# Optimization experiments

Measured on AMD Instinct MI355X. Metric: run time of the kernel, lower is better.

The kernel has to match this reference:

```python
import jax, jax.numpy as jnp
import numpy as np

# Qwen3-Next-like dims
B, S, HID = 2, 2048, 2048
H, KV, D, ROT = 16, 2, 128, 32
G = H // KV              # kv repeat groups
SCALE = D ** -0.5
EPS = 1e-6
BETA_BIAS, BIAS_CAP = 1.0, 3.0   # L1 logit bias
BETA_POST = 0.5                  # L2 post-softmax rescale
ALPHA_K, ALPHA_V = 0.1, 0.1      # L4 k/v rescale
GMIN, GMAX = 0.9, 1.1
EMIN, EMAX = 0.9, 1.1


def setup_inputs() -> dict:
    key = jax.random.key(0)
    ks = jax.random.split(key, 10)
    hidden_states = jax.random.normal(ks[0], (B, S, HID), jnp.float32)
    # partial rotary embeddings (rot_dim = head_dim // 4)
    pos = jnp.arange(S, dtype=jnp.float32)
    inv = 1.0 / (10000.0 ** (jnp.arange(0, ROT, 2, dtype=jnp.float32) / ROT))
    freqs = pos[:, None] * inv[None, :]
    emb = jnp.concatenate([freqs, freqs], axis=-1)          # [S, ROT]
    cos = jnp.broadcast_to(jnp.cos(emb)[None], (B, S, ROT)).astype(jnp.float32)
    sin = jnp.broadcast_to(jnp.sin(emb)[None], (B, S, ROT)).astype(jnp.float32)
    # additive causal mask [B,1,S,S]
    causal = jnp.tril(jnp.ones((S, S), jnp.bool_))
    attention_mask = jnp.where(causal, 0.0, -1e9).astype(jnp.float32)
    attention_mask = jnp.broadcast_to(attention_mask[None, None], (B, 1, S, S))
    # key prior: positive, sums to 1 over kv_len
    prior = jax.nn.softmax(jax.random.normal(ks[1], (S,), jnp.float32))
    s = 0.02
    Wq = jax.random.normal(ks[2], (HID, H * D * 2), jnp.float32) * s
    Wk = jax.random.normal(ks[3], (HID, KV * D), jnp.float32) * s
    Wv = jax.random.normal(ks[4], (HID, KV * D), jnp.float32) * s
    Wo = jax.random.normal(ks[5], (H * D, HID), jnp.float32) * s
    q_norm_w = 1.0 + 0.02 * jax.random.normal(ks[6], (D,), jnp.float32)
    k_norm_w = 1.0 + 0.02 * jax.random.normal(ks[7], (D,), jnp.float32)
    return {"hidden_states": hidden_states, "cos": cos, "sin": sin,
            "attention_mask": attention_mask, "prior": prior,
            "Wq": Wq, "Wk": Wk, "Wv": Wv, "Wo": Wo,
            "q_norm_w": q_norm_w, "k_norm_w": k_norm_w}


def _rms(x, w):
    return x * jax.lax.rsqrt(jnp.mean(x * x, axis=-1, keepdims=True) + EPS) * w


def _rot_half(x):
    x1, x2 = jnp.split(x, 2, axis=-1)
    return jnp.concatenate([-x2, x1], axis=-1)


def _rope(x, cos, sin):
    # x: [B,h,S,D]; rotary on first ROT dims only (Qwen3-Next partial rotary)
    xr, xp = x[..., :ROT], x[..., ROT:]
    xr = xr * cos + _rot_half(xr) * sin
    return jnp.concatenate([xr, xp], axis=-1)


def reference(hidden_states, cos, sin, attention_mask, prior, Wq, Wk, Wv, Wo, q_norm_w, k_norm_w):
    h = hidden_states
    # gated q projection: chunk into query + gate
    qg = (h @ Wq).reshape(B, S, H, 2 * D)
    q, gate = qg[..., :D], qg[..., D:]
    gate = gate.reshape(B, S, H * D)
    q = _rms(q, q_norm_w).transpose(0, 2, 1, 3)                       # [B,H,S,D]
    k = _rms((h @ Wk).reshape(B, S, KV, D), k_norm_w).transpose(0, 2, 1, 3)  # [B,KV,S,D]
    v = (h @ Wv).reshape(B, S, KV, D).transpose(0, 2, 1, 3)
    c, s_ = cos[:, None], sin[:, None]                                # [B,1,S,ROT]
    q, k = _rope(q, c, s_), _rope(k, c, s_)
    k = jnp.repeat(k, G, axis=1)                                      # GQA expand -> [B,H,S,D]
    v = jnp.repeat(v, G, axis=1)
    # L4: prior-based elementwise k/v rescale with clamped gamma/eta
    pc = prior * S                                                    # mean ~1 over keys
    gamma = jnp.clip(1.0 + ALPHA_K * (pc - 1.0), GMIN, GMAX)
    eta = jnp.clip(1.0 + ALPHA_V * (pc - 1.0), EMIN, EMAX)
    k = k * gamma[None, None, :, None]
    v = v * eta[None, None, :, None]
    scores = jnp.einsum('bhqd,bhkd->bhqk', q, k) * SCALE
    # L1: capped steering bias on logits
    scores = scores + jnp.clip(BETA_BIAS * prior, -BIAS_CAP, BIAS_CAP)[None, None, None, :]
    scores = scores + attention_mask
    probs = jax.nn.softmax(scores.astype(jnp.float32), axis=-1)       # fp32 softmax
    # L2: post-softmax prior rescale + renorm
    p2 = probs * (1.0 + BETA_POST * pc)[None, None, None, :]
    probs = p2 / jnp.sum(p2, axis=-1, keepdims=True)
    out = jnp.einsum('bhqk,bhkd->bhqd', probs.astype(h.dtype), v)
    out = out.transpose(0, 2, 1, 3).reshape(B, S, H * D)
    out = out * jax.nn.sigmoid(gate)                                  # gated attention output
    return out @ Wo
```

## Files before the change

kernel.cpp:

```cpp
#include <hip/hip_runtime.h>
#include <hip/hip_bf16.h>
#include <stdint.h>

#define B_    2
#define S_    2048
#define HID_  2048
#define H_    16
#define KV_   2
#define D_    128
#define ROT_  32
#define QGS   4608
#define SCALE_ 0.08838834764831845f

typedef __attribute__((ext_vector_type(8))) short  short8;
typedef __attribute__((ext_vector_type(4))) float  floatx4;

__device__ __forceinline__ float b2f(unsigned short u) {
  union { unsigned int i; float f; } v; v.i = ((unsigned int)u) << 16; return v.f;
}
__device__ __forceinline__ unsigned short f2b(float f) {
  union { float f; unsigned int i; } v; v.f = f;
  return (unsigned short)((v.i + 0x7fffu + ((v.i >> 16) & 1u)) >> 16);
}
__device__ __forceinline__ void gload_lds16(const unsigned short* g, unsigned short* l) {
  __builtin_amdgcn_global_load_lds((const __attribute__((address_space(1))) void*)g,
                                   (__attribute__((address_space(3))) void*)l, 16, 0, 0);
}

__device__ __forceinline__ void transpose_body(const float* __restrict__ in,
                                               unsigned short* __restrict__ out,
                                               int R, int C, int bx, int by, int t) {
  __shared__ unsigned short tile[64][68];
  int tx = t & 15, ty = t >> 4;
  long c0 = (long)bx * 64, r0 = (long)by * 64;
#pragma unroll
  for (int i = 0; i < 4; i++) {
    int row = ty + 16 * i;
    const float* src = in + (r0 + row) * C + c0 + 4 * tx;
    float4 v = *(const float4*)src;
    tile[row][4 * tx + 0] = f2b(v.x);
    tile[row][4 * tx + 1] = f2b(v.y);
    tile[row][4 * tx + 2] = f2b(v.z);
    tile[row][4 * tx + 3] = f2b(v.w);
  }
  __syncthreads();
#pragma unroll
  for (int i = 0; i < 4; i++) {
    int oc = ty + 16 * i;
    ushort4 v;
    v.x = tile[4 * tx + 0][oc];
    v.y = tile[4 * tx + 1][oc];
    v.z = tile[4 * tx + 2][oc];
    v.w = tile[4 * tx + 3][oc];
    *(ushort4*)(out + (c0 + oc) * R + r0 + 4 * tx) = v;
  }
}

__global__ __launch_bounds__(256) void k_preproc(const float* __restrict__ h_f,
                                                 const float* __restrict__ prior,
                                                 const float* __restrict__ Wq,
                                                 const float* __restrict__ Wk,
                                                 const float* __restrict__ Wv,
                                                 const float* __restrict__ Wo,
                                                 unsigned short* __restrict__ hb,
                                                 unsigned short* __restrict__ WqkvT,
                                                 unsigned short* __restrict__ WoT,
                                                 float* __restrict__ ge,
                                                 float* __restrict__ kbias) {
  int bx = blockIdx.x;
  const int t = threadIdx.x;
  if (bx < 8) {
    int i = bx * 256 + t;
    float p  = prior[i];
    float pc = p * (float)S_;
    float g  = 1.0f + 0.1f * (pc - 1.0f);
    g = fminf(fmaxf(g, 0.9f), 1.1f);
    ge[i] = g;
    float cb = fminf(fmaxf(p, -3.0f), 3.0f);
    kbias[i] = cb + logf(1.0f + 0.5f * pc);
    return;
  }
  bx -= 8;
  if (bx < 4096) {
    long i0 = ((long)bx * 256 + t) * 8;
    float4 a = *(const float4*)(h_f + i0);
    float4 b = *(const float4*)(h_f + i0 + 4);
    short8 v;
    v[0] = (short)f2b(a.x); v[1] = (short)f2b(a.y);
    v[2] = (short)f2b(a.z); v[3] = (short)f2b(a.w);
    v[4] = (short)f2b(b.x); v[5] = (short)f2b(b.y);
    v[6] = (short)f2b(b.z); v[7] = (short)f2b(b.w);
    *(short8*)(hb + i0) = v;
    return;
  }
  bx -= 4096;
  if (bx < 2048) { transpose_body(Wq, WqkvT, 2048, 4096, bx & 63, bx >> 6, t); return; }
  bx -= 2048;
  if (bx < 1024) { transpose_body(Wo, WoT, 2048, 2048, bx & 31, bx >> 5, t); return; }
  bx -= 1024;
  if (bx < 128)  { transpose_body(Wk, WqkvT + (size_t)4096 * 2048, 2048, 256, bx & 3, bx >> 2, t); return; }
  bx -= 128;
  transpose_body(Wv, WqkvT + (size_t)4352 * 2048, 2048, 256, bx & 3, bx >> 2, t);
}

template <int OUT32>
__global__ __launch_bounds__(256) void k_gemm_bt(const unsigned short* __restrict__ A,
                                                 const unsigned short* __restrict__ Bt,
                                                 void* __restrict__ Cv,
                                                 int M, int N, int K) {
  __shared__ __align__(16) unsigned short As[2][128 * 32];
  __shared__ __align__(16) unsigned short Bs[2][128 * 32];
  const int t    = threadIdx.x;
  const int lane = t & 63;
  const int wv   = t >> 6;
  const int wm   = wv >> 1, wn = wv & 1;
  const int nwg  = gridDim.x * gridDim.y;
  const int orig = blockIdx.y * gridDim.x + blockIdx.x;
  const int wg   = (orig & 7) * (nwg >> 3) + (orig >> 3);
  const int bxx  = wg % gridDim.x, byy = wg / gridDim.x;
  const long m0  = (long)byy * 128;
  const long n0  = (long)bxx * 128;
  const int r15  = lane & 15, g4 = lane >> 4;

  const int srow = lane >> 2;
  const int scol = ((lane & 3) ^ ((lane >> 3) & 3)) * 8;
  const unsigned short* sA0 = A  + (m0 + wv * 16 + srow)       * K + scol;
  const unsigned short* sA1 = A  + (m0 + (wv + 4) * 16 + srow) * K + scol;
  const unsigned short* sB0 = Bt + (n0 + wv * 16 + srow)       * K + scol;
  const unsigned short* sB1 = Bt + (n0 + (wv + 4) * 16 + srow) * K + scol;

  floatx4 acc[4][4];
#pragma unroll
  for (int m = 0; m < 4; m++)
#pragma unroll
    for (int n = 0; n < 4; n++) acc[m][n] = (floatx4){0.f, 0.f, 0.f, 0.f};

  gload_lds16(sA0, &As[0][wv * 512]);
  gload_lds16(sA1, &As[0][(wv + 4) * 512]);
  gload_lds16(sB0, &Bs[0][wv * 512]);
  gload_lds16(sB1, &Bs[0][(wv + 4) * 512]);
  __syncthreads();

  const int fcol = (g4 ^ ((r15 >> 1) & 3)) * 8;
  int cur = 0;
  for (int k0 = 0; k0 < K; k0 += 32) {
    if (k0 + 32 < K) {
      const int nx = cur ^ 1, ko = k0 + 32;
      gload_lds16(sA0 + ko, &As[nx][wv * 512]);
      gload_lds16(sA1 + ko, &As[nx][(wv + 4) * 512]);
      gload_lds16(sB0 + ko, &Bs[nx][wv * 512]);
      gload_lds16(sB1 + ko, &Bs[nx][(wv + 4) * 512]);
    }
    short8 af[4], bf[4];
#pragma unroll
    for (int m = 0; m < 4; m++)
      af[m] = *(const short8*)(&As[cur][(wm * 64 + m * 16 + r15) * 32 + fcol]);
#pragma unroll
    for (int n = 0; n < 4; n++)
      bf[n] = *(const short8*)(&Bs[cur][(wn * 64 + n * 16 + r15) * 32 + fcol]);
#pragma unroll
    for (int m = 0; m < 4; m++)
#pragma unroll
      for (int n = 0; n < 4; n++)
        acc[m][n] = __builtin_amdgcn_mfma_f32_16x16x32_bf16(af[m], bf[n], acc[m][n], 0, 0, 0);
    __syncthreads();
    cur ^= 1;
  }

#pragma unroll
  for (int m = 0; m < 4; m++) {
    const long rbase = m0 + wm * 64 + m * 16 + g4 * 4;
#pragma unroll
    for (int n = 0; n < 4; n++) {
      const long cidx = n0 + wn * 64 + n * 16 + r15;
#pragma unroll
      for (int i = 0; i < 4; i++) {
        if (OUT32) ((float*)Cv)[(rbase + i) * N + cidx] = acc[m][n][i];
        else ((unsigned short*)Cv)[(rbase + i) * N + cidx] = f2b(acc[m][n][i]);
      }
    }
  }
}

__global__ __launch_bounds__(256) void k_qkvpost(const unsigned short* __restrict__ qgkv,
                                                 const float* __restrict__ cosb,
                                                 const float* __restrict__ sinb,
                                                 const float* __restrict__ ge,
                                                 const float* __restrict__ knw,
                                                 unsigned short* __restrict__ kF,
                                                 unsigned short* __restrict__ vF) {
  int bxx = blockIdx.x;
  if (bxx < 2048) {
    int wid  = bxx * 4 + ((int)threadIdx.x >> 6);
    int lane = threadIdx.x & 63;
    int kvb  = wid & 1;
    long bs  = wid >> 1;
    int b = (int)(bs >> 11), s = (int)(bs & 2047);
    int d0 = lane * 2;

    const unsigned short* src = qgkv + bs * QGS + 4096 + kvb * 128 + d0;
    float x0 = b2f(src[0]), x1 = b2f(src[1]);
    float ss = x0 * x0 + x1 * x1;
#pragma unroll
    for (int mask = 1; mask < 64; mask <<= 1) ss += __shfl_xor(ss, mask);
    float rstd = rsqrtf(ss * (1.0f / 128.0f) + 1e-6f);
    float w0 = knw[d0], w1 = knw[d0 + 1];
    float xn0 = x0 * rstd * w0, xn1 = x1 * rstd * w1;
    float p0 = __shfl_xor(xn0, 8), p1 = __shfl_xor(xn1, 8);
    float y0 = xn0, y1 = xn1;
    if (lane < 16) {
      float c0 = cosb[bs * ROT_ + d0], c1 = cosb[bs * ROT_ + d0 + 1];
      float s0 = sinb[bs * ROT_ + d0], s1 = sinb[bs * ROT_ + d0 + 1];
      float sgn = (lane < 8) ? -1.0f : 1.0f;
      y0 = xn0 * c0 + sgn * p0 * s0;
      y1 = xn1 * c1 + sgn * p1 * s1;
    }
    float g = ge[s];
    unsigned int pack = (unsigned int)f2b(y0 * g) | ((unsigned int)f2b(y1 * g) << 16);
    size_t off = (size_t)(b * KV_ + kvb) * 262144
               + (size_t)((s >> 4) * 4 + (d0 >> 5)) * 512
               + (size_t)(((s & 15) + (((d0 >> 3) & 3)) * 16)) * 8 + (d0 & 7);
    *(unsigned int*)(kF + off) = pack;
  } else {
    int bx  = bxx - 2048;
    int scn = bx & 7, d = (bx >> 3) & 127, kvb = (bx >> 10) & 1, b = bx >> 11;
    int s = scn * 256 + threadIdx.x;
    float v = b2f(qgkv[((long)(b * S_ + s)) * QGS + 4352 + kvb * 128 + d]);
    v *= ge[s];
    size_t off = (size_t)(b * KV_ + kvb) * 262144
               + (size_t)((s >> 6) * 16 + (d >> 4) * 2 + ((s >> 5) & 1)) * 512
               + (size_t)((d & 15) + ((s >> 3) & 3) * 16) * 8 + (s & 7);
    vF[off] = f2b(v);
  }
}

__global__ __launch_bounds__(256) void k_attn(const unsigned short* __restrict__ qgkv,
                                              const unsigned short* __restrict__ kF,
                                              const unsigned short* __restrict__ vF,
                                              const float* __restrict__ kbias,
                                              const float* __restrict__ cosb,
                                              const float* __restrict__ sinb,
                                              const float* __restrict__ qnw,
                                              unsigned short* __restrict__ ag) {
  __shared__ __align__(16) unsigned short KL[2][8192];
  __shared__ __align__(16) unsigned short Ps[4][16 * 88];
  const int t = threadIdx.x;
  const int lane = t & 63, wv = t >> 6;
  const int r15 = lane & 15, g4 = lane >> 4;
  const int p = blockIdx.x;
  const int xcd = p & 7;
  const int grp = xcd >> 1;
  const int mem = ((p >> 3) << 1) | (xcd & 1);
  const int head = mem & 7;
  const int quad = 31 - (mem >> 3);
  const int b = grp >> 1, kvh = grp & 1;
  const int hh = kvh * 8 + head;
  const int strip = quad * 4 + wv;
  const int q0s = strip * 16;
  const int ntiles = quad + 1;

  const unsigned short* kFg = kF + (size_t)(b * KV_ + kvh) * 262144;
  const unsigned short* vFg = vF + (size_t)(b * KV_ + kvh) * 262144;

  short8 qf[4];
  {
    const int q = q0s + r15;
    const unsigned short* qp = qgkv + ((size_t)(b * S_) + q) * QGS + hh * 256 + g4 * 8;
    float xn[4][8];
    float ssq = 0.f;
#pragma unroll
    for (int kb = 0; kb < 4; kb++) {
      short8 qr = *(const short8*)(qp + kb * 32);
#pragma unroll
      for (int e = 0; e < 8; e++) {
        float x = b2f((unsigned short)qr[e]);
        xn[kb][e] = x;
        ssq += x * x;
      }
    }
    ssq += __shfl_xor(ssq, 16);
    ssq += __shfl_xor(ssq, 32);
    float rstd = rsqrtf(ssq * (1.0f / 128.0f) + 1e-6f);
#pragma unroll
    for (int kb = 0; kb < 4; kb++) {
      float4 w0 = *(const float4*)(&qnw[kb * 32 + g4 * 8]);
      float4 w1 = *(const float4*)(&qnw[kb * 32 + g4 * 8 + 4]);
      xn[kb][0] *= rstd * w0.x; xn[kb][1] *= rstd * w0.y;
      xn[kb][2] *= rstd * w0.z; xn[kb][3] *= rstd * w0.w;
      xn[kb][4] *= rstd * w1.x; xn[kb][5] *= rstd * w1.y;
      xn[kb][6] *= rstd * w1.z; xn[kb][7] *= rstd * w1.w;
    }
    {
      const float* cb = cosb + ((size_t)(b * S_) + q) * ROT_ + g4 * 8;
      const float* sb = sinb + ((size_t)(b * S_) + q) * ROT_ + g4 * 8;
      float4 c0 = *(const float4*)(cb), c1 = *(const float4*)(cb + 4);
      float4 s0 = *(const float4*)(sb), s1 = *(const float4*)(sb + 4);
      float cv[8] = {c0.x, c0.y, c0.z, c0.w, c1.x, c1.y, c1.z, c1.w};
      float sv[8] = {s0.x, s0.y, s0.z, s0.w, s1.x, s1.y, s1.z, s1.w};
      float sgn = (g4 < 2) ? -1.0f : 1.0f;
#pragma unroll
      for (int e = 0; e < 8; e++) {
        float part = __shfl_xor(xn[0][e], 32);
        xn[0][e] = xn[0][e] * cv[e] + sgn * part * sv[e];
      }
    }
#pragma unroll
    for (int kb = 0; kb < 4; kb++)
#pragma unroll
      for (int e = 0; e < 8; e++) qf[kb][e] = (short)f2b(xn[kb][e]);
  }

  floatx4 oacc[8];
#pragma unroll
  for (int nd = 0; nd < 8; nd++) oacc[nd] = (floatx4){0.f, 0.f, 0.f, 0.f};
  float mrow = -1e30f, lrw = 0.f;

#pragma unroll
  for (int i = 0; i < 4; i++)
    gload_lds16(kFg + (size_t)wv * 2048 + i * 512 + lane * 8, &KL[0][wv * 2048 + i * 512]);
  __syncthreads();

  int cur = 0;
  for (int tile = 0; tile < ntiles; tile++) {
    if (tile + 1 < ntiles) {
      const size_t src = (size_t)(tile + 1) * 8192 + wv * 2048 + lane * 8;
#pragma unroll
      for (int i = 0; i < 4; i++)
        gload_lds16(kFg + src + i * 512, &KL[cur ^ 1][wv * 2048 + i * 512]);
    }

    floatx4 sacc[4];
#pragma unroll
    for (int n = 0; n < 4; n++) sacc[n] = (floatx4){0.f, 0.f, 0.f, 0.f};
    __builtin_amdgcn_s_setprio(1);
#pragma unroll
    for (int n = 0; n < 4; n++) {
      const unsigned short* kl = &KL[cur][n * 2048 + lane * 8];
      short8 a0 = *(const short8*)(kl);
      short8 a1 = *(const short8*)(kl + 512);
      short8 a2 = *(const short8*)(kl + 1024);
      short8 a3 = *(const short8*)(kl + 1536);
      sacc[n] = __builtin_amdgcn_mfma_f32_16x16x32_bf16(a0, qf[0], sacc[n], 0, 0, 0);
      sacc[n] = __builtin_amdgcn_mfma_f32_16x16x32_bf16(a1, qf[1], sacc[n], 0, 0, 0);
      sacc[n] = __builtin_amdgcn_mfma_f32_16x16x32_bf16(a2, qf[2], sacc[n], 0, 0, 0);
      sacc[n] = __builtin_amdgcn_mfma_f32_16x16x32_bf16(a3, qf[3], sacc[n], 0, 0, 0);
    }
    __builtin_amdgcn_s_setprio(0);

    const unsigned short* vt = vFg + (size_t)tile * 8192 + lane * 8;
    short8 vfA[8];
#pragma unroll
    for (int nd = 0; nd < 8; nd++) vfA[nd] = *(const short8*)(vt + (nd * 2) * 512);

    const bool last = (tile == ntiles - 1);
    float scf[4][4];
#pragma unroll
    for (int n = 0; n < 4; n++) {
      const int j0 = tile * 64;
      float4 kb4 = *(const float4*)(&kbias[j0 + n * 16 + g4 * 4]);
#pragma unroll
      for (int i = 0; i < 4; i++) {
        float kbv = (i == 0) ? kb4.x : (i == 1) ? kb4.y : (i == 2) ? kb4.z : kb4.w;
        float v = sacc[n][i] * SCALE_ + kbv;
        if (last) {
          int jg = j0 + n * 16 + g4 * 4 + i;
          if (jg > q0s + r15) v = -1e30f;
        }
        scf[n][i] = v;
      }
    }
    float pmax = scf[0][0];
#pragma unroll
    for (int n = 0; n < 4; n++)
#pragma unroll
      for (int i = 0; i < 4; i++) pmax = fmaxf(pmax, scf[n][i]);
    pmax = fmaxf(pmax, __shfl_xor(pmax, 16));
    pmax = fmaxf(pmax, __shfl_xor(pmax, 32));
    if (__any(pmax > mrow + 8.0f)) {
      float mn = fmaxf(mrow, pmax);
      float aq = __expf(mrow - mn);
      mrow = mn;
      lrw *= aq;
      float ai[4];
#pragma unroll
      for (int i = 0; i < 4; i++) ai[i] = __shfl(aq, g4 * 4 + i);
#pragma unroll
      for (int nd = 0; nd < 8; nd++)
#pragma unroll
        for (int i = 0; i < 4; i++) oacc[nd][i] *= ai[i];
    }
    float rsum = 0.f;
#pragma unroll
    for (int n = 0; n < 4; n++)
#pragma unroll
      for (int i = 0; i < 4; i++) {
        float pv = __expf(scf[n][i] - mrow);
        scf[n][i] = pv;
        rsum += pv;
      }
    rsum += __shfl_xor(rsum, 16);
    rsum += __shfl_xor(rsum, 32);
    lrw += rsum;

#pragma unroll
    for (int n = 0; n < 4; n++) {
      unsigned int lo = (unsigned int)f2b(scf[n][0]) | ((unsigned int)f2b(scf[n][1]) << 16);
      unsigned int hi = (unsigned int)f2b(scf[n][2]) | ((unsigned int)f2b(scf[n][3]) << 16);
      uint2 w; w.x = lo; w.y = hi;
      *(uint2*)(&Ps[wv][r15 * 88 + n * 16 + g4 * 4]) = w;
    }

    short8 vfB[8];
#pragma unroll
    for (int nd = 0; nd < 8; nd++) vfB[nd] = *(const short8*)(vt + (nd * 2 + 1) * 512);

    {
      __builtin_amdgcn_s_setprio(1);
      short8 pa0 = *(const short8*)(&Ps[wv][r15 * 88 + g4 * 8]);
#pragma unroll
      for (int nd = 0; nd < 8; nd++)
        oacc[nd] = __builtin_amdgcn_mfma_f32_16x16x32_bf16(pa0, vfA[nd], oacc[nd], 0, 0, 0);
      short8 pa1 = *(const short8*)(&Ps[wv][r15 * 88 + 32 + g4 * 8]);
#pragma unroll
      for (int nd = 0; nd < 8; nd++)
        oacc[nd] = __builtin_amdgcn_mfma_f32_16x16x32_bf16(pa1, vfB[nd], oacc[nd], 0, 0, 0);
      __builtin_amdgcn_s_setprio(0);
    }
    __syncthreads();
    cur ^= 1;
  }

  float il[4];
#pragma unroll
  for (int i = 0; i < 4; i++) il[i] = __shfl(lrw, g4 * 4 + i);
#pragma unroll
  for (int i = 0; i < 4; i++) {
    int q = q0s + g4 * 4 + i;
    float inv = 1.0f / il[i];
    const unsigned short* gptr = qgkv + ((size_t)(b * S_ + q)) * QGS + hh * 256 + 128;
    unsigned short* aptr = ag + ((size_t)(b * S_ + q)) * (H_ * D_) + hh * D_;
#pragma unroll
    for (int nd = 0; nd < 8; nd++) {
      int d = nd * 16 + r15;
      float gt = b2f(gptr[d]);
      float sg = 1.0f / (1.0f + __expf(-gt));
      aptr[d] = f2b(oacc[nd][i] * inv * sg);
    }
  }
}

extern "C" void kernel_launch(void* const* d_in, const int* in_sizes, int n_in,
                              void* d_out, int out_size, void* d_ws, size_t ws_size,
                              hipStream_t stream) {
  const float* h_f   = (const float*)d_in[0];
  const float* cosb  = (const float*)d_in[1];
  const float* sinb  = (const float*)d_in[2];
  const float* prior = (const float*)d_in[4];
  const float* Wq    = (const float*)d_in[5];
  const float* Wk    = (const float*)d_in[6];
  const float* Wv    = (const float*)d_in[7];
  const float* Wo    = (const float*)d_in[8];
  const float* qnw   = (const float*)d_in[9];
  const float* knw   = (const float*)d_in[10];

  char* ws = (char*)d_ws;
  size_t off = 0;
  auto alloc = [&](size_t bytes) { char* p = ws + off; off += (bytes + 255) & ~(size_t)255; return p; };
  unsigned short* hb    = (unsigned short*)alloc((size_t)4096 * 2048 * 2);
  unsigned short* WqkvT = (unsigned short*)alloc((size_t)4608 * 2048 * 2);
  unsigned short* WoT   = (unsigned short*)alloc((size_t)2048 * 2048 * 2);
  unsigned short* qgkv  = (unsigned short*)alloc((size_t)4096 * QGS * 2);
  unsigned short* kF    = (unsigned short*)alloc((size_t)B_ * KV_ * S_ * D_ * 2);
  unsigned short* vF    = (unsigned short*)alloc((size_t)B_ * KV_ * S_ * D_ * 2);
  float* ge    = (float*)alloc((size_t)S_ * 4);
  float* kbias = (float*)alloc((size_t)S_ * 4);
  unsigned short* ag = hb;

  dim3 blk(256);
  k_preproc<<<dim3(7432), blk, 0, stream>>>(h_f, prior, Wq, Wk, Wv, Wo,
                                            hb, WqkvT, WoT, ge, kbias);
  k_gemm_bt<0><<<dim3(36, 32), blk, 0, stream>>>(hb, WqkvT, qgkv, 4096, QGS, 2048);
  k_qkvpost<<<dim3(6144), blk, 0, stream>>>(qgkv, cosb, sinb, ge, knw, kF, vF);
  k_attn<<<dim3(1024), blk, 0, stream>>>(qgkv, kF, vF, kbias, cosb, sinb, qnw, ag);
  k_gemm_bt<1><<<dim3(16, 32), blk, 0, stream>>>(ag, WoT, d_out, 4096, 2048, 2048);
}
```

Measured before the change: 268.6 us.

## Triple-buffer GEMM LDS tiles with one barrier per k-step and vmcnt waits

Replaces the GEMM's double-buffered LDS pipeline with a three-stage ring buffer. Loads run two k-tiles ahead, gated by explicit s_waitcnt vmcnt counts and a single s_barrier per iteration instead of a trailing __syncthreads. It also drops the XCD-aware workgroup remapping in favour of plain blockIdx tiling. The aim is to hide global-to-LDS latency better, at the cost of 50% more LDS, which may lower occupancy, and possibly worse L2 locality across XCDs. The cos/sin pointer variables in the attention kernel are renamed to avoid a clash with the new name.

```diff
diff --git a/kernel.cpp b/kernel.cpp
--- a/kernel.cpp
+++ b/kernel.cpp
@@ -108,18 +108,14 @@
                                                  const unsigned short* __restrict__ Bt,
                                                  void* __restrict__ Cv,
                                                  int M, int N, int K) {
-  __shared__ __align__(16) unsigned short As[2][128 * 32];
-  __shared__ __align__(16) unsigned short Bs[2][128 * 32];
+  __shared__ __align__(16) unsigned short As[3][128 * 32];
+  __shared__ __align__(16) unsigned short Bs[3][128 * 32];
   const int t    = threadIdx.x;
   const int lane = t & 63;
   const int wv   = t >> 6;
   const int wm   = wv >> 1, wn = wv & 1;
-  const int nwg  = gridDim.x * gridDim.y;
-  const int orig = blockIdx.y * gridDim.x + blockIdx.x;
-  const int wg   = (orig & 7) * (nwg >> 3) + (orig >> 3);
-  const int bxx  = wg % gridDim.x, byy = wg / gridDim.x;
-  const long m0  = (long)byy * 128;
-  const long n0  = (long)bxx * 128;
+  const long m0  = (long)blockIdx.y * 128;
+  const long n0  = (long)blockIdx.x * 128;
   const int r15  = lane & 15, g4 = lane >> 4;
 
   const int srow = lane >> 2;
@@ -135,36 +131,45 @@
 #pragma unroll
     for (int n = 0; n < 4; n++) acc[m][n] = (floatx4){0.f, 0.f, 0.f, 0.f};
 
-  gload_lds16(sA0, &As[0][wv * 512]);
-  gload_lds16(sA1, &As[0][(wv + 4) * 512]);
-  gload_lds16(sB0, &Bs[0][wv * 512]);
-  gload_lds16(sB1, &Bs[0][(wv + 4) * 512]);
-  __syncthreads();
+  const int nk = K >> 5;
+#pragma unroll
+  for (int kt = 0; kt < 2; kt++) {
+    const int ko = kt * 32;
+    gload_lds16(sA0 + ko, &As[kt][wv * 512]);
+    gload_lds16(sA1 + ko, &As[kt][(wv + 4) * 512]);
+    gload_lds16(sB0 + ko, &Bs[kt][wv * 512]);
+    gload_lds16(sB1 + ko, &Bs[kt][(wv + 4) * 512]);
+  }
 
   const int fcol = (g4 ^ ((r15 >> 1) & 3)) * 8;
-  int cur = 0;
-  for (int k0 = 0; k0 < K; k0 += 32) {
-    if (k0 + 32 < K) {
-      const int nx = cur ^ 1, ko = k0 + 32;
-      gload_lds16(sA0 + ko, &As[nx][wv * 512]);
-      gload_lds16(sA1 + ko, &As[nx][(wv + 4) * 512]);
-      gload_lds16(sB0 + ko, &Bs[nx][wv * 512]);
-      gload_lds16(sB1 + ko, &Bs[nx][(wv + 4) * 512]);
+  int cb = 0;
+  for (int k = 0; k < nk; ++k) {
+    if (k < nk - 1) asm volatile("s_waitcnt vmcnt(4)" ::: "memory");
+    else            asm volatile("s_waitcnt vmcnt(0)" ::: "memory");
+    __builtin_amdgcn_sched_barrier(0);
+    __builtin_amdgcn_s_barrier();
+    __builtin_amdgcn_sched_barrier(0);
+    if (k + 2 < nk) {
+      const int nb = (cb + 2 >= 3) ? cb - 1 : cb + 2;
+      const int ko = (k + 2) * 32;
+      gload_lds16(sA0 + ko, &As[nb][wv * 512]);
+      gload_lds16(sA1 + ko, &As[nb][(wv + 4) * 512]);
+      gload_lds16(sB0 + ko, &Bs[nb][wv * 512]);
+      gload_lds16(sB1 + ko, &Bs[nb][(wv + 4) * 512]);
     }
     short8 af[4], bf[4];
 #pragma unroll
     for (int m = 0; m < 4; m++)
-      af[m] = *(const short8*)(&As[cur][(wm * 64 + m * 16 + r15) * 32 + fcol]);
+      af[m] = *(const short8*)(&As[cb][(wm * 64 + m * 16 + r15) * 32 + fcol]);
 #pragma unroll
     for (int n = 0; n < 4; n++)
-      bf[n] = *(const short8*)(&Bs[cur][(wn * 64 + n * 16 + r15) * 32 + fcol]);
+      bf[n] = *(const short8*)(&Bs[cb][(wn * 64 + n * 16 + r15) * 32 + fcol]);
 #pragma unroll
     for (int m = 0; m < 4; m++)
 #pragma unroll
       for (int n = 0; n < 4; n++)
         acc[m][n] = __builtin_amdgcn_mfma_f32_16x16x32_bf16(af[m], bf[n], acc[m][n], 0, 0, 0);
-    __syncthreads();
-    cur ^= 1;
+    cb = (cb == 2) ? 0 : cb + 1;
   }
 
 #pragma unroll
@@ -291,10 +296,10 @@
       xn[kb][6] *= rstd * w1.z; xn[kb][7] *= rstd * w1.w;
     }
     {
-      const float* cb = cosb + ((size_t)(b * S_) + q) * ROT_ + g4 * 8;
-      const float* sb = sinb + ((size_t)(b * S_) + q) * ROT_ + g4 * 8;
-      float4 c0 = *(const float4*)(cb), c1 = *(const float4*)(cb + 4);
-      float4 s0 = *(const float4*)(sb), s1 = *(const float4*)(sb + 4);
+      const float* cbp = cosb + ((size_t)(b * S_) + q) * ROT_ + g4 * 8;
+      const float* sbp = sinb + ((size_t)(b * S_) + q) * ROT_ + g4 * 8;
+      float4 c0 = *(const float4*)(cbp), c1 = *(const float4*)(cbp + 4);
+      float4 s0 = *(const float4*)(sbp), s1 = *(const float4*)(sbp + 4);
       float cv[8] = {c0.x, c0.y, c0.z, c0.w, c1.x, c1.y, c1.z, c1.w};
       float sv[8] = {s0.x, s0.y, s0.z, s0.w, s1.x, s1.y, s1.z, s1.w};
       float sgn = (g4 < 2) ? -1.0f : 1.0f;
```

Measured after the change: 260.6 us. 3.0% less time.
